# Kernel tuning notes

Measured on AMD Instinct MI355X. Metric: run time of the kernel, lower is better.

Reference implementation:

```python
import jax, jax.numpy as jnp
import numpy as np

EPS = 1e-6

def gram_schmidt_orthonormalize(U, eps=EPS):
    # U: [B, K, D] -> orthonormalized along K, vectorized over batch
    B, K, D = U.shape
    vs = []
    for i in range(K):
        v = U[:, i]  # [B, D]
        for vj in vs:
            coeff = jnp.sum(v * vj, axis=1, keepdims=True) / (jnp.sum(vj * vj, axis=1, keepdims=True) + eps)
            v = v - coeff * vj
        norm = jnp.maximum(jnp.linalg.norm(v, axis=1, keepdims=True), eps)
        vs.append(v / norm)
    return jnp.stack(vs, axis=1)  # [B, K, D]

def setup_inputs() -> dict:
    key = jax.random.key(0)
    ks = jax.random.split(key, 14)
    B, IN, H1, H2, OUT, E, G = 4096, 1024, 2048, 2048, 512, 8, 256
    s = 0.02
    return {
        "x":   jax.random.normal(ks[0], (B, IN), jnp.float32),
        "W1":  jax.random.normal(ks[1], (E, IN, H1), jnp.float32) * s,
        "b1":  jnp.zeros((E, H1), jnp.float32),
        "W2":  jax.random.normal(ks[2], (E, H1, H2), jnp.float32) * s,
        "b2":  jnp.zeros((E, H2), jnp.float32),
        "W3":  jax.random.normal(ks[3], (E, H2, OUT), jnp.float32) * s,
        "b3":  jnp.zeros((E, OUT), jnp.float32),
        "Wg1": jax.random.normal(ks[4], (IN, G), jnp.float32) * s,
        "bg1": jnp.zeros((G,), jnp.float32),
        "Wg2": jax.random.normal(ks[5], (G, E), jnp.float32) * s,
        "bg2": jnp.zeros((E,), jnp.float32),
        "Wo":  jax.random.normal(ks[6], (OUT, 1), jnp.float32) * s,
        "bo":  jnp.zeros((1,), jnp.float32),
    }

def reference(x, W1, b1, W2, b2, W3, b3, Wg1, bg1, Wg2, bg2, Wo, bo):
    # Expert MLPs, batched over expert axis e: [B,E,h]
    h = jax.nn.relu(jnp.einsum('bi,eih->beh', x, W1) + b1)
    h = jax.nn.relu(jnp.einsum('beh,ehk->bek', h, W2) + b2)
    expert_outputs = jnp.einsum('bek,ekd->bed', h, W3) + b3  # [B, E, D]
    # Gating network: MLP + softmax over experts
    g = jax.nn.relu(x @ Wg1 + bg1)
    gate_weights = jax.nn.softmax(g @ Wg2 + bg2, axis=-1)  # [B, E]
    # Per-sample Gram-Schmidt across experts, weighted combine
    ortho = gram_schmidt_orthonormalize(expert_outputs)  # [B, E, D]
    combined = jnp.einsum('bed,be->bd', ortho, gate_weights)  # [B, D]
    final = combined @ Wo + bo  # [B, 1]
    return (final, 0.0)
```

## Files before the change

kernel.cpp:

```cpp
#include <hip/hip_runtime.h>
#include <hip/hip_bf16.h>

#define DEVINL __device__ __forceinline__

constexpr int Bsz = 4096, INF = 1024, H1 = 2048, H2 = 2048, OUTD = 512, NE = 8, G = 256;

typedef __attribute__((ext_vector_type(8))) short bf16x8;
typedef __attribute__((ext_vector_type(4))) float f32x4;

DEVINL unsigned short f2bf(float f) {
  unsigned int u = __float_as_uint(f);
  u = (u + 0x7FFFu + ((u >> 16) & 1u)) >> 16;
  return (unsigned short)u;
}
DEVINL float bf2f(unsigned short h) { return __uint_as_float((unsigned int)h << 16); }

DEVINL void gload16(const void* g, void* l) {
  __builtin_amdgcn_global_load_lds(
      (const __attribute__((address_space(1))) void*)g,
      (__attribute__((address_space(3))) void*)l, 16, 0, 0);
}

DEVINL float waveAllSum(float v) {
#pragma unroll
  for (int m = 32; m > 0; m >>= 1) v += __shfl_xor(v, m, 64);
  return v;
}

__global__ __launch_bounds__(256) void pack_act(const float* __restrict__ in,
                                                unsigned short* __restrict__ hi,
                                                unsigned short* __restrict__ lo) {
  size_t i = ((size_t)blockIdx.x * 256 + threadIdx.x) * 4;
  float4 v = *(const float4*)&in[i];
  short4 h, l;
  h.x = f2bf(v.x); l.x = f2bf(v.x - bf2f(h.x));
  h.y = f2bf(v.y); l.y = f2bf(v.y - bf2f(h.y));
  h.z = f2bf(v.z); l.z = f2bf(v.z - bf2f(h.z));
  h.w = f2bf(v.w); l.w = f2bf(v.w - bf2f(h.w));
  *(short4*)&hi[i] = h;
  *(short4*)&lo[i] = l;
}

__global__ __launch_bounds__(256) void pack_wt(const float* __restrict__ W,
                                               unsigned short* __restrict__ Th,
                                               unsigned short* __restrict__ Tl,
                                               int K, int N) {
  __shared__ float t[32][33];
  const int e = blockIdx.z;
  W += (size_t)e * K * N;
  Th += (size_t)e * N * K;
  Tl += (size_t)e * N * K;
  const int n0 = blockIdx.x * 32, k0 = blockIdx.y * 32;
  const int r = threadIdx.x >> 3, c = (threadIdx.x & 7) * 4;
  float4 v = *(const float4*)&W[(size_t)(k0 + r) * N + n0 + c];
  t[r][c + 0] = v.x; t[r][c + 1] = v.y; t[r][c + 2] = v.z; t[r][c + 3] = v.w;
  __syncthreads();
  float o0 = t[c + 0][r], o1 = t[c + 1][r], o2 = t[c + 2][r], o3 = t[c + 3][r];
  short4 h, l;
  h.x = f2bf(o0); l.x = f2bf(o0 - bf2f(h.x));
  h.y = f2bf(o1); l.y = f2bf(o1 - bf2f(h.y));
  h.z = f2bf(o2); l.z = f2bf(o2 - bf2f(h.z));
  h.w = f2bf(o3); l.w = f2bf(o3 - bf2f(h.w));
  *(short4*)&Th[(size_t)(n0 + r) * K + k0 + c] = h;
  *(short4*)&Tl[(size_t)(n0 + r) * K + k0 + c] = l;
}

template <int RELU, int OUTF32>
__global__ __launch_bounds__(512) void gemm_bf16x3_256(
    const unsigned short* __restrict__ Ahi, const unsigned short* __restrict__ Alo,
    const unsigned short* __restrict__ Bhi, const unsigned short* __restrict__ Blo,
    const float* __restrict__ bias,
    unsigned short* __restrict__ Chi, unsigned short* __restrict__ Clo,
    float* __restrict__ Cf, int M, int N, int K, size_t strideAe) {
  const int e = blockIdx.z;
  Ahi += (size_t)e * strideAe;
  Alo += (size_t)e * strideAe;
  Bhi += (size_t)e * (size_t)N * K;
  Blo += (size_t)e * (size_t)N * K;
  bias += (size_t)e * N;
  if (OUTF32) Cf += (size_t)e * (size_t)M * N;
  else { Chi += (size_t)e * (size_t)M * N; Clo += (size_t)e * (size_t)M * N; }

  const int bm = blockIdx.y * 256, bn = blockIdx.x * 256;
  __shared__ char ldsb[2 * 65536];
  const int lane = threadIdx.x & 63, wid = threadIdx.x >> 6;
  const int wm = wid >> 2, wn = wid & 3;
  const int l15 = lane & 15, l4 = lane >> 4;

  const int sec = wid >> 1, half = wid & 1;
  const unsigned short* sb = (sec == 0) ? Ahi : (sec == 1) ? Alo : (sec == 2) ? Bhi : Blo;
  const int t0 = (sec < 2) ? bm : bn;
  const unsigned short* gp0 = sb + (size_t)(t0 + half * 128 + l15) * K + l4 * 8;
  char* ldsw = ldsb + sec * 16384 + half * 8192;

  f32x4 acc[8][4];
#pragma unroll
  for (int i = 0; i < 8; ++i)
#pragma unroll
    for (int j = 0; j < 4; ++j) acc[i][j] = (f32x4){0.f, 0.f, 0.f, 0.f};

#pragma unroll
  for (int f = 0; f < 8; ++f)
    gload16(gp0 + (size_t)(f * 16) * K, ldsw + f * 1024);

  int cur = 0;
  for (int k0 = 0; k0 < K; k0 += 32) {
    __syncthreads();
    if (k0 + 32 < K) {
      const unsigned short* gp = gp0 + k0 + 32;
      char* dst = ldsw + (cur ^ 1) * 65536;
#pragma unroll
      for (int f = 0; f < 8; ++f)
        gload16(gp + (size_t)(f * 16) * K, dst + f * 1024);
    }
    const char* rb = ldsb + cur * 65536;
    bf16x8 bh[4], bl[4];
#pragma unroll
    for (int j = 0; j < 4; ++j) {
      bh[j] = *(const bf16x8*)(rb + 32768 + (wn * 4 + j) * 1024 + lane * 16);
      bl[j] = *(const bf16x8*)(rb + 49152 + (wn * 4 + j) * 1024 + lane * 16);
    }
#pragma unroll
    for (int i = 0; i < 8; ++i) {
      bf16x8 ah = *(const bf16x8*)(rb + (wm * 8 + i) * 1024 + lane * 16);
      bf16x8 al = *(const bf16x8*)(rb + 16384 + (wm * 8 + i) * 1024 + lane * 16);
#pragma unroll
      for (int j = 0; j < 4; ++j) {
        acc[i][j] = __builtin_amdgcn_mfma_f32_16x16x32_bf16(bh[j], ah, acc[i][j], 0, 0, 0);
        acc[i][j] = __builtin_amdgcn_mfma_f32_16x16x32_bf16(bl[j], ah, acc[i][j], 0, 0, 0);
        acc[i][j] = __builtin_amdgcn_mfma_f32_16x16x32_bf16(bh[j], al, acc[i][j], 0, 0, 0);
      }
    }
    cur ^= 1;
  }

#pragma unroll
  for (int i = 0; i < 8; ++i) {
    const int grow = bm + wm * 128 + i * 16 + l15;
#pragma unroll
    for (int j = 0; j < 4; ++j) {
      const int gcol = bn + wn * 64 + j * 16 + l4 * 4;
      const float4 bb = *(const float4*)&bias[gcol];
      float v0 = acc[i][j][0] + bb.x, v1 = acc[i][j][1] + bb.y;
      float v2 = acc[i][j][2] + bb.z, v3 = acc[i][j][3] + bb.w;
      if (RELU) {
        v0 = fmaxf(v0, 0.f); v1 = fmaxf(v1, 0.f);
        v2 = fmaxf(v2, 0.f); v3 = fmaxf(v3, 0.f);
      }
      if (OUTF32) {
        *(float4*)&Cf[(size_t)grow * N + gcol] = make_float4(v0, v1, v2, v3);
      } else {
        short4 h, l;
        h.x = f2bf(v0); l.x = f2bf(v0 - bf2f(h.x));
        h.y = f2bf(v1); l.y = f2bf(v1 - bf2f(h.y));
        h.z = f2bf(v2); l.z = f2bf(v2 - bf2f(h.z));
        h.w = f2bf(v3); l.w = f2bf(v3 - bf2f(h.w));
        *(short4*)&Chi[(size_t)grow * N + gcol] = h;
        *(short4*)&Clo[(size_t)grow * N + gcol] = l;
      }
    }
  }
}

__global__ __launch_bounds__(256) void gate1_kernel(
    const float* __restrict__ x, const float* __restrict__ Wg1,
    const float* __restrict__ bg1, float* __restrict__ g) {
  __shared__ float xs[8 * 1024];
  const int b0 = blockIdx.x * 8;
  const float* xp = x + (size_t)b0 * INF;
  for (int idx = threadIdx.x * 4; idx < 8 * 1024; idx += 1024)
    *(float4*)&xs[idx] = *(const float4*)&xp[idx];
  __syncthreads();
  const int t = threadIdx.x;
  float acc[8] = {0, 0, 0, 0, 0, 0, 0, 0};
  for (int i = 0; i < INF; ++i) {
    float w = Wg1[(size_t)i * G + t];
#pragma unroll
    for (int r = 0; r < 8; ++r) acc[r] = fmaf(xs[r * 1024 + i], w, acc[r]);
  }
  const float bb = bg1[t];
#pragma unroll
  for (int r = 0; r < 8; ++r)
    g[(size_t)(b0 + r) * G + t] = fmaxf(acc[r] + bb, 0.0f);
}

__global__ __launch_bounds__(64) void gate2_kernel(
    const float* __restrict__ g, const float* __restrict__ Wg2,
    const float* __restrict__ bg2, float* __restrict__ gw) {
  const int b = blockIdx.x, lane = threadIdx.x;
  float4 gv = *(const float4*)(g + (size_t)b * G + lane * 4);
  float p[8];
#pragma unroll
  for (int e = 0; e < 8; ++e) {
    int j = lane * 4;
    float s = gv.x * Wg2[(j + 0) * 8 + e] + gv.y * Wg2[(j + 1) * 8 + e] +
              gv.z * Wg2[(j + 2) * 8 + e] + gv.w * Wg2[(j + 3) * 8 + e];
    p[e] = waveAllSum(s);
  }
  if (lane == 0) {
    float l[8];
    float mx = -1e30f;
#pragma unroll
    for (int e = 0; e < 8; ++e) {
      l[e] = p[e] + bg2[e];
      mx = fmaxf(mx, l[e]);
    }
    float sum = 0.0f;
#pragma unroll
    for (int e = 0; e < 8; ++e) {
      l[e] = expf(l[e] - mx);
      sum += l[e];
    }
    float inv = 1.0f / sum;
#pragma unroll
    for (int e = 0; e < 8; ++e) gw[(size_t)b * 8 + e] = l[e] * inv;
  }
}

__global__ __launch_bounds__(256) void gs_kernel(
    const float* __restrict__ eo, const float* __restrict__ gw,
    const float* __restrict__ Wo, const float* __restrict__ bo,
    float* __restrict__ out, int CB) {
  const int lane = threadIdx.x & 63;
  const int b = blockIdx.x * 4 + (threadIdx.x >> 6);
  const size_t ES = (size_t)CB * OUTD;
  const float* base = eo + (size_t)b * OUTD + lane * 8;
  float vs[8][8];
  float denom[8];
#pragma unroll
  for (int i = 0; i < 8; ++i) {
    float cur[8];
    float4 u0 = *(const float4*)(base + (size_t)i * ES);
    float4 u1 = *(const float4*)(base + (size_t)i * ES + 4);
    cur[0] = u0.x; cur[1] = u0.y; cur[2] = u0.z; cur[3] = u0.w;
    cur[4] = u1.x; cur[5] = u1.y; cur[6] = u1.z; cur[7] = u1.w;
#pragma unroll
    for (int j = 0; j < i; ++j) {
      float dp = 0.0f;
#pragma unroll
      for (int d = 0; d < 8; ++d) dp = fmaf(cur[d], vs[j][d], dp);
      dp = waveAllSum(dp);
      float coeff = dp / (denom[j] + 1e-6f);
#pragma unroll
      for (int d = 0; d < 8; ++d) cur[d] = fmaf(-coeff, vs[j][d], cur[d]);
    }
    float nn = 0.0f;
#pragma unroll
    for (int d = 0; d < 8; ++d) nn = fmaf(cur[d], cur[d], nn);
    nn = waveAllSum(nn);
    float inv = 1.0f / fmaxf(sqrtf(nn), 1e-6f);
#pragma unroll
    for (int d = 0; d < 8; ++d) vs[i][d] = cur[d] * inv;
    float dd = 0.0f;
#pragma unroll
    for (int d = 0; d < 8; ++d) dd = fmaf(vs[i][d], vs[i][d], dd);
    denom[i] = waveAllSum(dd);
  }
  float gwv[8];
#pragma unroll
  for (int e = 0; e < 8; ++e) gwv[e] = gw[(size_t)b * 8 + e];
  float part = 0.0f;
#pragma unroll
  for (int d = 0; d < 8; ++d) {
    float c = 0.0f;
#pragma unroll
    for (int e = 0; e < 8; ++e) c = fmaf(vs[e][d], gwv[e], c);
    part = fmaf(c, Wo[lane * 8 + d], part);
  }
  part = waveAllSum(part);
  if (lane == 0) out[b] = part + bo[0];
}

extern "C" void kernel_launch(void* const* d_in, const int* in_sizes, int n_in,
                              void* d_out, int out_size, void* d_ws, size_t ws_size,
                              hipStream_t stream) {
  const float* x   = (const float*)d_in[0];
  const float* W1  = (const float*)d_in[1];
  const float* b1  = (const float*)d_in[2];
  const float* W2  = (const float*)d_in[3];
  const float* b2  = (const float*)d_in[4];
  const float* W3  = (const float*)d_in[5];
  const float* b3  = (const float*)d_in[6];
  const float* Wg1 = (const float*)d_in[7];
  const float* bg1 = (const float*)d_in[8];
  const float* Wg2 = (const float*)d_in[9];
  const float* bg2 = (const float*)d_in[10];
  const float* Wo  = (const float*)d_in[11];
  const float* bo  = (const float*)d_in[12];
  float* out = (float*)d_out;

  typedef unsigned short u16;
  char* p = (char*)d_ws;
  float* gw = (float*)p;          p += (size_t)(128u << 10);
  float* g  = (float*)p;          p += (size_t)(4u << 20);
  u16* xhi = (u16*)p;             p += (size_t)Bsz * INF * 2;
  u16* xlo = (u16*)p;             p += (size_t)Bsz * INF * 2;
  u16* w1h = (u16*)p;             p += (size_t)NE * H1 * INF * 2;
  u16* w1l = (u16*)p;             p += (size_t)NE * H1 * INF * 2;
  u16* w2h = (u16*)p;             p += (size_t)NE * H2 * H1 * 2;
  u16* w2l = (u16*)p;             p += (size_t)NE * H2 * H1 * 2;
  u16* w3h = (u16*)p;             p += (size_t)NE * OUTD * H2 * 2;
  u16* w3l = (u16*)p;             p += (size_t)NE * OUTD * H2 * 2;
  const size_t fixedBytes = (size_t)(p - (char*)d_ws);

  int CB = 4096;
  while (CB > 256 && fixedBytes + (size_t)CB * (size_t)(128u << 10) > ws_size) CB >>= 1;
  u16* h1h = (u16*)p;
  u16* h1l = h1h + (size_t)NE * CB * H1;
  u16* h2h = h1l + (size_t)NE * CB * H1;
  u16* h2l = h2h + (size_t)NE * CB * H2;
  float* eo = (float*)h1h;

  hipMemsetAsync(d_out, 0, (size_t)out_size * sizeof(float), stream);

  pack_act<<<(Bsz * INF) / 1024, 256, 0, stream>>>(x, xhi, xlo);
  pack_wt<<<dim3(H1 / 32, INF / 32, NE), 256, 0, stream>>>(W1, w1h, w1l, INF, H1);
  pack_wt<<<dim3(H2 / 32, H1 / 32, NE), 256, 0, stream>>>(W2, w2h, w2l, H1, H2);
  pack_wt<<<dim3(OUTD / 32, H2 / 32, NE), 256, 0, stream>>>(W3, w3h, w3l, H2, OUTD);

  gate1_kernel<<<Bsz / 8, 256, 0, stream>>>(x, Wg1, bg1, g);
  gate2_kernel<<<Bsz, 64, 0, stream>>>(g, Wg2, bg2, gw);

  for (int c0 = 0; c0 < Bsz; c0 += CB) {
    gemm_bf16x3_256<1, 0><<<dim3(H1 / 256, CB / 256, NE), 512, 0, stream>>>(
        xhi + (size_t)c0 * INF, xlo + (size_t)c0 * INF, w1h, w1l, b1,
        h1h, h1l, nullptr, CB, H1, INF, (size_t)0);
    gemm_bf16x3_256<1, 0><<<dim3(H2 / 256, CB / 256, NE), 512, 0, stream>>>(
        h1h, h1l, w2h, w2l, b2, h2h, h2l, nullptr, CB, H2, H1, (size_t)CB * H1);
    gemm_bf16x3_256<0, 1><<<dim3(OUTD / 256, CB / 256, NE), 512, 0, stream>>>(
        h2h, h2l, w3h, w3l, b3, nullptr, nullptr, eo, CB, OUTD, H2, (size_t)CB * H2);
    gs_kernel<<<CB / 4, 256, 0, stream>>>(eo, gw + (size_t)c0 * NE, Wo, bo,
                                          out + c0, CB);
  }
}
```

Baseline: 1.737 ms.

## Deepen GEMM prefetch pipeline with split-phase MFMA and expert-major grid order

Restructures the bf16x3 GEMM main loop so two K-tiles are in flight. Explicit vmcnt/lgkmcnt waits and raw s_barrier calls replace __syncthreads. Each iteration is split into two halves so the next global-to-LDS prefetch is issued mid-iteration, and s_setprio raises wave priority around the MFMA bursts. It also reorders the launch grid so the expert index varies fastest, which changes which blocks run concurrently and may alter L2 reuse of activations and weights. The manual waitcnt and barrier scheduling is fragile and adds an extra barrier per tile.

```diff
diff --git a/kernel.cpp b/kernel.cpp
--- a/kernel.cpp
+++ b/kernel.cpp
@@ -66,13 +66,13 @@
 }
 
 template <int RELU, int OUTF32>
-__global__ __launch_bounds__(512) void gemm_bf16x3_256(
+__global__ __launch_bounds__(512, 1) void gemm_bf16x3_256(
     const unsigned short* __restrict__ Ahi, const unsigned short* __restrict__ Alo,
     const unsigned short* __restrict__ Bhi, const unsigned short* __restrict__ Blo,
     const float* __restrict__ bias,
     unsigned short* __restrict__ Chi, unsigned short* __restrict__ Clo,
     float* __restrict__ Cf, int M, int N, int K, size_t strideAe) {
-  const int e = blockIdx.z;
+  const int e = blockIdx.x;
   Ahi += (size_t)e * strideAe;
   Alo += (size_t)e * strideAe;
   Bhi += (size_t)e * (size_t)N * K;
@@ -81,7 +81,7 @@
   if (OUTF32) Cf += (size_t)e * (size_t)M * N;
   else { Chi += (size_t)e * (size_t)M * N; Clo += (size_t)e * (size_t)M * N; }
 
-  const int bm = blockIdx.y * 256, bn = blockIdx.x * 256;
+  const int bm = blockIdx.y * 256, bn = blockIdx.z * 256;
   __shared__ char ldsb[2 * 65536];
   const int lane = threadIdx.x & 63, wid = threadIdx.x >> 6;
   const int wm = wid >> 2, wn = wid & 3;
@@ -99,21 +99,77 @@
 #pragma unroll
     for (int j = 0; j < 4; ++j) acc[i][j] = (f32x4){0.f, 0.f, 0.f, 0.f};
 
+  const int nt = K / 32;
 #pragma unroll
   for (int f = 0; f < 8; ++f)
     gload16(gp0 + (size_t)(f * 16) * K, ldsw + f * 1024);
-
-  int cur = 0;
-  for (int k0 = 0; k0 < K; k0 += 32) {
-    __syncthreads();
-    if (k0 + 32 < K) {
-      const unsigned short* gp = gp0 + k0 + 32;
-      char* dst = ldsw + (cur ^ 1) * 65536;
+#pragma unroll
+  for (int f = 0; f < 8; ++f)
+    gload16(gp0 + 32 + (size_t)(f * 16) * K, ldsw + 65536 + f * 1024);
+
+  for (int t = 0; t < nt - 1; ++t) {
+    const int cur = t & 1;
+    asm volatile("s_waitcnt vmcnt(8)" ::: "memory");
+    __builtin_amdgcn_sched_barrier(0);
+    __builtin_amdgcn_s_barrier();
+    __builtin_amdgcn_sched_barrier(0);
+    const char* rb = ldsb + cur * 65536;
+    bf16x8 bh[4], bl[4], a0h[4], a0l[4];
+#pragma unroll
+    for (int j = 0; j < 4; ++j) {
+      bh[j] = *(const bf16x8*)(rb + 32768 + (wn * 4 + j) * 1024 + lane * 16);
+      bl[j] = *(const bf16x8*)(rb + 49152 + (wn * 4 + j) * 1024 + lane * 16);
+    }
+#pragma unroll
+    for (int i = 0; i < 4; ++i) {
+      a0h[i] = *(const bf16x8*)(rb + (wm * 8 + i) * 1024 + lane * 16);
+      a0l[i] = *(const bf16x8*)(rb + 16384 + (wm * 8 + i) * 1024 + lane * 16);
+    }
+    __builtin_amdgcn_s_setprio(1);
+#pragma unroll
+    for (int i = 0; i < 4; ++i)
+#pragma unroll
+      for (int j = 0; j < 4; ++j) {
+        acc[i][j] = __builtin_amdgcn_mfma_f32_16x16x32_bf16(bh[j], a0h[i], acc[i][j], 0, 0, 0);
+        acc[i][j] = __builtin_amdgcn_mfma_f32_16x16x32_bf16(bl[j], a0h[i], acc[i][j], 0, 0, 0);
+        acc[i][j] = __builtin_amdgcn_mfma_f32_16x16x32_bf16(bh[j], a0l[i], acc[i][j], 0, 0, 0);
+      }
+    __builtin_amdgcn_s_setprio(0);
+    bf16x8 a1h[4], a1l[4];
+#pragma unroll
+    for (int i = 0; i < 4; ++i) {
+      a1h[i] = *(const bf16x8*)(rb + (wm * 8 + 4 + i) * 1024 + lane * 16);
+      a1l[i] = *(const bf16x8*)(rb + 16384 + (wm * 8 + 4 + i) * 1024 + lane * 16);
+    }
+    asm volatile("s_waitcnt lgkmcnt(0)" ::: "memory");
+    __builtin_amdgcn_sched_barrier(0);
+    __builtin_amdgcn_s_barrier();
+    __builtin_amdgcn_sched_barrier(0);
+    if (t + 2 < nt) {
+      const unsigned short* gp = gp0 + (t + 2) * 32;
+      char* dst = ldsw + cur * 65536;
 #pragma unroll
       for (int f = 0; f < 8; ++f)
         gload16(gp + (size_t)(f * 16) * K, dst + f * 1024);
     }
-    const char* rb = ldsb + cur * 65536;
+    __builtin_amdgcn_s_setprio(1);
+#pragma unroll
+    for (int i = 0; i < 4; ++i)
+#pragma unroll
+      for (int j = 0; j < 4; ++j) {
+        acc[4 + i][j] = __builtin_amdgcn_mfma_f32_16x16x32_bf16(bh[j], a1h[i], acc[4 + i][j], 0, 0, 0);
+        acc[4 + i][j] = __builtin_amdgcn_mfma_f32_16x16x32_bf16(bl[j], a1h[i], acc[4 + i][j], 0, 0, 0);
+        acc[4 + i][j] = __builtin_amdgcn_mfma_f32_16x16x32_bf16(bh[j], a1l[i], acc[4 + i][j], 0, 0, 0);
+      }
+    __builtin_amdgcn_s_setprio(0);
+  }
+
+  asm volatile("s_waitcnt vmcnt(0)" ::: "memory");
+  __builtin_amdgcn_sched_barrier(0);
+  __builtin_amdgcn_s_barrier();
+  __builtin_amdgcn_sched_barrier(0);
+  {
+    const char* rb = ldsb + ((nt - 1) & 1) * 65536;
     bf16x8 bh[4], bl[4];
 #pragma unroll
     for (int j = 0; j < 4; ++j) {
@@ -131,7 +187,6 @@
         acc[i][j] = __builtin_amdgcn_mfma_f32_16x16x32_bf16(bh[j], al, acc[i][j], 0, 0, 0);
       }
     }
-    cur ^= 1;
   }
 
 #pragma unroll
@@ -322,12 +377,12 @@
   gate2_kernel<<<Bsz, 64, 0, stream>>>(g, Wg2, bg2, gw);
 
   for (int c0 = 0; c0 < Bsz; c0 += CB) {
-    gemm_bf16x3_256<1, 0><<<dim3(H1 / 256, CB / 256, NE), 512, 0, stream>>>(
+    gemm_bf16x3_256<1, 0><<<dim3(NE, CB / 256, H1 / 256), 512, 0, stream>>>(
         xhi + (size_t)c0 * INF, xlo + (size_t)c0 * INF, w1h, w1l, b1,
         h1h, h1l, nullptr, CB, H1, INF, (size_t)0);
-    gemm_bf16x3_256<1, 0><<<dim3(H2 / 256, CB / 256, NE), 512, 0, stream>>>(
+    gemm_bf16x3_256<1, 0><<<dim3(NE, CB / 256, H2 / 256), 512, 0, stream>>>(
         h1h, h1l, w2h, w2l, b2, h2h, h2l, nullptr, CB, H2, H1, (size_t)CB * H1);
-    gemm_bf16x3_256<0, 1><<<dim3(OUTD / 256, CB / 256, NE), 512, 0, stream>>>(
+    gemm_bf16x3_256<0, 1><<<dim3(NE, CB / 256, OUTD / 256), 512, 0, stream>>>(
         h2h, h2l, w3h, w3l, b3, nullptr, nullptr, eo, CB, OUTD, H2, (size_t)CB * H2);
     gs_kernel<<<CB / 4, 256, 0, stream>>>(eo, gw + (size_t)c0 * NE, Wo, bo,
                                           out + c0, CB);
```

New measurement: 1.776 ms. 2.3% more time.

## Restructure bf16x3 GEMM main loop into four-phase pipelined schedule with staggered loads

Applied to the files above, without the earlier changes.

Rewrites the GEMM inner loop as four MFMA quadrants per k-step, each separated by barriers, with global-to-LDS loads for A (one step ahead) and B (two steps ahead) spread across the phases and explicit vmcnt waits. It also raises MFMA priority with s_setprio during the compute phases and changes the grid so the expert index sits in blockIdx.x, which alters block scheduling order and L2 locality. The aim is to overlap memory traffic with matrix math and hide LDS read latency. It adds more barriers per k-step and relies on hand-counted waitcnt values, and launch_bounds(512,2) with 128KB of LDS may limit occupancy or force register spills.

```diff
diff --git a/kernel.cpp b/kernel.cpp
--- a/kernel.cpp
+++ b/kernel.cpp
@@ -65,14 +65,35 @@
   *(short4*)&Tl[(size_t)(n0 + r) * K + k0 + c] = l;
 }
 
+#define PHASE_MID()                                    \
+  __builtin_amdgcn_sched_barrier(0);                   \
+  __builtin_amdgcn_s_barrier();                        \
+  asm volatile("s_waitcnt lgkmcnt(0)" ::: "memory");   \
+  __builtin_amdgcn_sched_barrier(0)
+#define PHASE_END()                                    \
+  __builtin_amdgcn_sched_barrier(0);                   \
+  __builtin_amdgcn_s_barrier()
+#define QUAD(IH, JH, BH, BL)                                                   \
+  __builtin_amdgcn_s_setprio(1);                                               \
+  _Pragma("unroll") for (int i = 0; i < 4; ++i) {                              \
+    _Pragma("unroll") for (int j = 0; j < 2; ++j) {                            \
+      f32x4 a = acc[(IH)*4 + i][(JH)*2 + j];                                   \
+      a = __builtin_amdgcn_mfma_f32_16x16x32_bf16(BH[j], ah[i], a, 0, 0, 0);   \
+      a = __builtin_amdgcn_mfma_f32_16x16x32_bf16(BL[j], ah[i], a, 0, 0, 0);   \
+      a = __builtin_amdgcn_mfma_f32_16x16x32_bf16(BH[j], al[i], a, 0, 0, 0);   \
+      acc[(IH)*4 + i][(JH)*2 + j] = a;                                         \
+    }                                                                          \
+  }                                                                            \
+  __builtin_amdgcn_s_setprio(0);
+
 template <int RELU, int OUTF32>
-__global__ __launch_bounds__(512) void gemm_bf16x3_256(
+__global__ __launch_bounds__(512, 2) void gemm_bf16x3_8ph(
     const unsigned short* __restrict__ Ahi, const unsigned short* __restrict__ Alo,
     const unsigned short* __restrict__ Bhi, const unsigned short* __restrict__ Blo,
     const float* __restrict__ bias,
     unsigned short* __restrict__ Chi, unsigned short* __restrict__ Clo,
     float* __restrict__ Cf, int M, int N, int K, size_t strideAe) {
-  const int e = blockIdx.z;
+  const int e = blockIdx.x;
   Ahi += (size_t)e * strideAe;
   Alo += (size_t)e * strideAe;
   Bhi += (size_t)e * (size_t)N * K;
@@ -81,17 +102,12 @@
   if (OUTF32) Cf += (size_t)e * (size_t)M * N;
   else { Chi += (size_t)e * (size_t)M * N; Clo += (size_t)e * (size_t)M * N; }
 
-  const int bm = blockIdx.y * 256, bn = blockIdx.x * 256;
-  __shared__ char ldsb[2 * 65536];
+  const int bm = blockIdx.y * 256, bn = blockIdx.z * 256;
+  __shared__ __align__(16) char ldsb[131072];
   const int lane = threadIdx.x & 63, wid = threadIdx.x >> 6;
   const int wm = wid >> 2, wn = wid & 3;
   const int l15 = lane & 15, l4 = lane >> 4;
-
-  const int sec = wid >> 1, half = wid & 1;
-  const unsigned short* sb = (sec == 0) ? Ahi : (sec == 1) ? Alo : (sec == 2) ? Bhi : Blo;
-  const int t0 = (sec < 2) ? bm : bn;
-  const unsigned short* gp0 = sb + (size_t)(t0 + half * 128 + l15) * K + l4 * 8;
-  char* ldsw = ldsb + sec * 16384 + half * 8192;
+  const int bhalf = wn >> 1, jn = wn & 1;
 
   f32x4 acc[8][4];
 #pragma unroll
@@ -99,39 +115,78 @@
 #pragma unroll
     for (int j = 0; j < 4; ++j) acc[i][j] = (f32x4){0.f, 0.f, 0.f, 0.f};
 
-#pragma unroll
-  for (int f = 0; f < 8; ++f)
-    gload16(gp0 + (size_t)(f * 16) * K, ldsw + f * 1024);
-
-  int cur = 0;
-  for (int k0 = 0; k0 < K; k0 += 32) {
-    __syncthreads();
-    if (k0 + 32 < K) {
-      const unsigned short* gp = gp0 + k0 + 32;
-      char* dst = ldsw + (cur ^ 1) * 65536;
-#pragma unroll
-      for (int f = 0; f < 8; ++f)
-        gload16(gp + (size_t)(f * 16) * K, dst + f * 1024);
-    }
-    const char* rb = ldsb + cur * 65536;
-    bf16x8 bh[4], bl[4];
-#pragma unroll
-    for (int j = 0; j < 4; ++j) {
-      bh[j] = *(const bf16x8*)(rb + 32768 + (wn * 4 + j) * 1024 + lane * 16);
-      bl[j] = *(const bf16x8*)(rb + 49152 + (wn * 4 + j) * 1024 + lane * 16);
-    }
-#pragma unroll
-    for (int i = 0; i < 8; ++i) {
-      bf16x8 ah = *(const bf16x8*)(rb + (wm * 8 + i) * 1024 + lane * 16);
-      bf16x8 al = *(const bf16x8*)(rb + 16384 + (wm * 8 + i) * 1024 + lane * 16);
-#pragma unroll
-      for (int j = 0; j < 4; ++j) {
-        acc[i][j] = __builtin_amdgcn_mfma_f32_16x16x32_bf16(bh[j], ah, acc[i][j], 0, 0, 0);
-        acc[i][j] = __builtin_amdgcn_mfma_f32_16x16x32_bf16(bl[j], ah, acc[i][j], 0, 0, 0);
-        acc[i][j] = __builtin_amdgcn_mfma_f32_16x16x32_bf16(bh[j], al, acc[i][j], 0, 0, 0);
-      }
-    }
-    cur ^= 1;
+  const int nt = K / 32;
+
+  auto stageA = [&](const unsigned short* src, int T, int ldsOp) {
+    const int s = T & 1;
+#pragma unroll
+    for (int q = 0; q < 2; ++q) {
+      const int g = wid * 2 + q;
+      gload16(src + (size_t)(bm + g * 16 + l15) * K + T * 32 + l4 * 8,
+              ldsb + ldsOp + s * 16384 + g * 1024);
+    }
+  };
+  auto stageB = [&](int T, int h) {
+    const int s = T & 1;
+#pragma unroll
+    for (int q = 0; q < 2; ++q) {
+      const int g = wid * 2 + q;
+      const unsigned short* src = (g < 8) ? Bhi : Blo;
+      const int f = g & 7;
+      gload16(src + (size_t)(bn + h * 128 + f * 16 + l15) * K + T * 32 + l4 * 8,
+              ldsb + ((g < 8) ? 65536 : 98304) + s * 16384 + h * 8192 + f * 1024);
+    }
+  };
+
+  bf16x8 ah[4], al[4], b0h[2], b0l[2], b1h[2], b1l[2];
+  auto readA = [&](int s, int ih) {
+#pragma unroll
+    for (int i = 0; i < 4; ++i) {
+      const int off = s * 16384 + wm * 8192 + (ih * 4 + i) * 1024 + lane * 16;
+      ah[i] = *(const bf16x8*)(ldsb + off);
+      al[i] = *(const bf16x8*)(ldsb + 32768 + off);
+    }
+  };
+  auto readB = [&](int s, int jh, bf16x8* bh, bf16x8* bl) {
+#pragma unroll
+    for (int j = 0; j < 2; ++j) {
+      const int off = s * 16384 + bhalf * 8192 + (jn * 4 + jh * 2 + j) * 1024 + lane * 16;
+      bh[j] = *(const bf16x8*)(ldsb + 65536 + off);
+      bl[j] = *(const bf16x8*)(ldsb + 98304 + off);
+    }
+  };
+
+  stageB(0, 0); stageB(0, 1);
+  stageA(Ahi, 0, 0); stageA(Alo, 0, 32768);
+  stageB(1, 0); stageB(1, 1);
+  asm volatile("s_waitcnt vmcnt(4)" ::: "memory");
+  __builtin_amdgcn_sched_barrier(0);
+  __builtin_amdgcn_s_barrier();
+
+  for (int t = 0; t < nt; ++t) {
+    const int s = t & 1;
+    readA(s, 0);
+    readB(s, 0, b0h, b0l);
+    if (t + 1 < nt) stageA(Ahi, t + 1, 0);
+    PHASE_MID();
+    QUAD(0, 0, b0h, b0l);
+    PHASE_END();
+    readB(s, 1, b1h, b1l);
+    if (t + 1 < nt) stageA(Alo, t + 1, 32768);
+    PHASE_MID();
+    QUAD(0, 1, b1h, b1l);
+    PHASE_END();
+    readA(s, 1);
+    if (t + 2 < nt) stageB(t + 2, 0);
+    PHASE_MID();
+    QUAD(1, 0, b0h, b0l);
+    PHASE_END();
+    if (t + 2 < nt) stageB(t + 2, 1);
+    PHASE_MID();
+    QUAD(1, 1, b1h, b1l);
+    asm volatile("s_waitcnt vmcnt(4)" ::: "memory");
+    __builtin_amdgcn_sched_barrier(0);
+    PHASE_END();
   }
 
 #pragma unroll
@@ -322,12 +377,12 @@
   gate2_kernel<<<Bsz, 64, 0, stream>>>(g, Wg2, bg2, gw);
 
   for (int c0 = 0; c0 < Bsz; c0 += CB) {
-    gemm_bf16x3_256<1, 0><<<dim3(H1 / 256, CB / 256, NE), 512, 0, stream>>>(
+    gemm_bf16x3_8ph<1, 0><<<dim3(NE, CB / 256, H1 / 256), 512, 0, stream>>>(
         xhi + (size_t)c0 * INF, xlo + (size_t)c0 * INF, w1h, w1l, b1,
         h1h, h1l, nullptr, CB, H1, INF, (size_t)0);
-    gemm_bf16x3_256<1, 0><<<dim3(H2 / 256, CB / 256, NE), 512, 0, stream>>>(
+    gemm_bf16x3_8ph<1, 0><<<dim3(NE, CB / 256, H2 / 256), 512, 0, stream>>>(
         h1h, h1l, w2h, w2l, b2, h2h, h2l, nullptr, CB, H2, H1, (size_t)CB * H1);
-    gemm_bf16x3_256<0, 1><<<dim3(OUTD / 256, CB / 256, NE), 512, 0, stream>>>(
+    gemm_bf16x3_8ph<0, 1><<<dim3(NE, CB / 256, OUTD / 256), 512, 0, stream>>>(
         h2h, h2l, w3h, w3l, b3, nullptr, nullptr, eo, CB, OUTD, H2, (size_t)CB * H2);
     gs_kernel<<<CB / 4, 256, 0, stream>>>(eo, gw + (size_t)c0 * NE, Wo, bo,
                                           out + c0, CB);
```

New measurement: 1.617 ms. 6.9% less time.
